# Kernel tuning notes

Hardware: AMD Instinct MI355X
Metric: run time of the kernel (lower is better)

The kernel has to match this reference:

```python
import jax, jax.numpy as jnp
import numpy as np

D = 1024       # d_model
H = 16         # num_heads
DK = D // H    # head dim (64)
DFF = 4096     # SwiGLU hidden dim
THETA = 10000.0
EPS = 1e-5
B, S = 2, 2048


def setup_inputs() -> dict:
    key = jax.random.key(0)
    ks = jax.random.split(key, 9)
    p = lambda k, shape: jax.random.normal(k, shape, dtype=jnp.float32) * 0.02
    return {
        "x": jax.random.normal(ks[0], (B, S, D), dtype=jnp.float32),
        "w_q": p(ks[1], (D, D)),   # Linear stores [out, in]
        "w_k": p(ks[2], (D, D)),
        "w_v": p(ks[3], (D, D)),
        "w_o": p(ks[4], (D, D)),
        "ln1_w": jnp.ones((D,), dtype=jnp.float32),
        "ln2_w": jnp.ones((D,), dtype=jnp.float32),
        "w1": p(ks[5], (DFF, D)),  # gate-in proj: d_model -> dff
        "w2": p(ks[6], (D, DFF)),  # down proj:    dff -> d_model
        "w3": p(ks[7], (DFF, D)),  # up proj:      d_model -> dff
    }


def _rmsnorm(x, w):
    xf = x.astype(jnp.float32)
    inv = jax.lax.rsqrt(jnp.mean(xf * xf, axis=-1, keepdims=True) + EPS)
    return (inv * xf * w).astype(x.dtype)


def _rope(x, pos):
    # x: [..., seq, DK]; pos: [seq]
    inv_freq = THETA ** (-(jnp.arange(0, DK, 2, dtype=jnp.float32) / DK))  # [DK/2]
    ang = pos.astype(jnp.float32)[:, None] * inv_freq                      # [seq, DK/2]
    cos, sin = jnp.cos(ang), jnp.sin(ang)
    xe, xo = x[..., ::2], x[..., 1::2]
    re = cos * xe - sin * xo
    ro = sin * xe + cos * xo
    return jnp.stack((re, ro), axis=-1).reshape(x.shape)  # interleave even/odd


def reference(x, w_q, w_k, w_v, w_o, ln1_w, ln2_w, w1, w2, w3):
    b, s, d = x.shape
    pos = jnp.arange(s)

    # --- attention sublayer ---
    h = _rmsnorm(x, ln1_w)
    def proj(w):  # [b,s,d] x [d,d] -> [b,H,s,DK]
        return jnp.einsum('bsd,ed->bse', h, w).reshape(b, s, H, DK).transpose(0, 2, 1, 3)
    q = _rope(proj(w_q), pos)
    k = _rope(proj(w_k), pos)
    v = proj(w_v)

    scores = jnp.einsum('bhqd,bhkd->bhqk', q, k) / (DK ** 0.5)
    causal = jnp.tril(jnp.ones((s, s), dtype=bool))
    scores = jnp.where(causal, scores, -jnp.inf)
    attn = jax.nn.softmax(scores, axis=-1)
    o = jnp.einsum('bhqk,bhkd->bhqd', attn, v).transpose(0, 2, 1, 3).reshape(b, s, d)
    x = x + jnp.einsum('bsd,ed->bse', o, w_o)

    # --- SwiGLU FFN sublayer ---
    h2 = _rmsnorm(x, ln2_w)
    u = jnp.einsum('bsd,fd->bsf', h2, w1)
    g = jnp.einsum('bsd,fd->bsf', h2, w3)
    ffn = jnp.einsum('bsf,df->bsd', u * jax.nn.sigmoid(u) * g, w2)
    return x + ffn
```

## Files before the change

### kernel.cpp

```cpp
#include <hip/hip_runtime.h>

typedef _Float16 half_t;
typedef _Float16 f16x8 __attribute__((ext_vector_type(8)));
typedef _Float16 f16x4 __attribute__((ext_vector_type(4)));
typedef _Float16 f16x2 __attribute__((ext_vector_type(2)));
typedef float fx4 __attribute__((ext_vector_type(4)));

typedef __attribute__((address_space(1))) const unsigned int as1_cuint;
typedef __attribute__((address_space(3))) unsigned int as3_uint;

__device__ __forceinline__ void gld16(const void* g, void* l) {
    __builtin_amdgcn_global_load_lds((as1_cuint*)g, (as3_uint*)l, 16, 0, 0);
}

template<int MODE>
__global__ __launch_bounds__(256, 2)
void gemm_bt(const half_t* __restrict__ A,
             const half_t* __restrict__ B0, const half_t* __restrict__ B1,
             const half_t* __restrict__ B2,
             half_t* o0, half_t* o1, half_t* o2, half_t* o3,
             int M, int N, int K)
{
    __shared__ half_t sA[128 * 32];
    __shared__ half_t sB[128 * 32];
    const int tid = threadIdx.x;
    const int wid = tid >> 6, lane = tid & 63;
    const int lm = lane & 15, lg = lane >> 4;
    const int wr = wid >> 1, wc = wid & 1;
    const int m0 = blockIdx.x * 128, n0 = blockIdx.y * 128;

    const half_t* Bp = B0;
    half_t* outb = o0;
    if (MODE == 1) {
        if (blockIdx.z == 1) { Bp = B1; outb = o1; }
        else if (blockIdx.z == 2) { Bp = B2; outb = o2; }
    }
    if (MODE == 4) {
        if (blockIdx.z == 1) outb = o1;
        else if (blockIdx.z == 2) outb = o2;
        else if (blockIdx.z == 3) outb = o3;
    }

    int Keff = K, koff = 0;
    if (MODE == 4) { Keff = K / gridDim.z; koff = blockIdx.z * Keff; }

    const int srow = tid >> 2;
    const int scolb = ((tid & 3) ^ ((srow >> 1) & 3)) << 4;
    const char* gA = (const char*)(A + (size_t)(m0 + srow) * K + koff) + scolb;
    const char* gB = (const char*)(Bp + (size_t)(n0 + srow) * K + koff) + scolb;
    const size_t rstep = (size_t)64 * K * sizeof(half_t);
    char* lA = (char*)sA + tid * 16;
    char* lB = (char*)sB + tid * 16;

    const int ksw = (lm >> 1) & 3;

    fx4 acc[4][4] = {};

    for (int kt = 0; kt < Keff; kt += 32) {
        gld16(gA, lA);
        gld16(gA + rstep, lA + 4096);
        gld16(gB, lB);
        gld16(gB + rstep, lB + 4096);
        gA += 64; gB += 64;
        __syncthreads();
        f16x8 aF[4], bF[4];
#pragma unroll
        for (int mi = 0; mi < 4; mi++)
            aF[mi] = *(const f16x8*)(sA + (wr * 64 + mi * 16 + lm) * 32 + (lg ^ ksw) * 8);
#pragma unroll
        for (int ni = 0; ni < 4; ni++)
            bF[ni] = *(const f16x8*)(sB + (wc * 64 + ni * 16 + lm) * 32 + (lg ^ ksw) * 8);
#pragma unroll
        for (int mi = 0; mi < 4; mi++)
#pragma unroll
            for (int ni = 0; ni < 4; ni++)
                acc[mi][ni] = __builtin_amdgcn_mfma_f32_16x16x32_f16(aF[mi], bF[ni], acc[mi][ni], 0, 0, 0);
        __syncthreads();
    }

#pragma unroll
    for (int mi = 0; mi < 4; mi++) {
#pragma unroll
        for (int ni = 0; ni < 4; ni++) {
#pragma unroll
            for (int r = 0; r < 4; r++) {
                int m = m0 + wr * 64 + mi * 16 + lg * 4 + r;
                int n = n0 + wc * 64 + ni * 16 + lm;
                float v = acc[mi][ni][r];
                size_t idx = (size_t)m * N + n;
                if (MODE == 1) {
                    int b = m >> 11, s = m & 2047, hh = n >> 6, dk = n & 63;
                    if (blockIdx.z == 2) {
                        outb[((size_t)(b * 16 + hh) * 64 + dk) * 2048 + s] = (half_t)v;
                    } else {
                        float pv = __shfl_xor(v, 1);
                        float f = __expf((float)(dk >> 1) * -0.28782313662f);
                        float c, sn;
                        __sincosf((float)s * f, &sn, &c);
                        float xe = (lm & 1) ? pv : v;
                        float xo = (lm & 1) ? v : pv;
                        float rv = (lm & 1) ? (sn * xe + c * xo) : (c * xe - sn * xo);
                        if (blockIdx.z == 0) rv *= 0.125f;
                        outb[((size_t)(b * 16 + hh) * 2048 + s) * 64 + dk] = (half_t)rv;
                    }
                } else {
                    outb[idx] = (half_t)v;
                }
            }
        }
    }
}

#define L256(buf, half, sec) (lbase + (buf) * 65536 + (half) * 16384 + (sec) * 8192)

#define KT256(CUR)                                                            \
  {                                                                           \
    const int BO = (CUR) * 65536;                                             \
    const int st1 = (t < nt - 1), st2 = (t < nt - 2);                         \
    const int s1 = (t + 1) * 128, s2 = (t + 2) * 128;                         \
    f16x8 aLo[4][2], aHi[4][2], bA[2][2], bB[2][2];                           \
                                         \
    _Pragma("unroll") for (int mi = 0; mi < 4; mi++) {                        \
        aLo[mi][0] = *(const f16x8*)(aBase + BO + mi * 2048 + swz0);          \
        aLo[mi][1] = *(const f16x8*)(aBase + BO + mi * 2048 + swz1);          \
    }                                                                         \
    _Pragma("unroll") for (int ni = 0; ni < 2; ni++) {                        \
        bA[ni][0] = *(const f16x8*)(bBase + BO + ni * 2048 + swz0);           \
        bA[ni][1] = *(const f16x8*)(bBase + BO + ni * 2048 + swz1);           \
    }                                                                         \
    if (st1) { gld16(pB10 + s1, L256(1 - (CUR), 3, 0));                       \
               gld16(pB1h + s1, L256(1 - (CUR), 3, 1)); }                     \
    asm volatile("s_waitcnt lgkmcnt(8)" ::: "memory");                        \
    __builtin_amdgcn_s_barrier();                                             \
    asm volatile("s_waitcnt lgkmcnt(0)" ::: "memory");                        \
    __builtin_amdgcn_sched_barrier(0);                                        \
    __builtin_amdgcn_s_setprio(1);                                            \
    _Pragma("unroll") for (int kk = 0; kk < 2; kk++)                          \
      _Pragma("unroll") for (int mi = 0; mi < 4; mi++)                        \
        _Pragma("unroll") for (int ni = 0; ni < 2; ni++)                      \
          acc[mi][ni] = __builtin_amdgcn_mfma_f32_16x16x32_f16(aLo[mi][kk], bA[ni][kk], acc[mi][ni], 0, 0, 0); \
    __builtin_amdgcn_s_setprio(0);                                            \
    __builtin_amdgcn_s_barrier();                                             \
                                         \
    _Pragma("unroll") for (int ni = 0; ni < 2; ni++) {                        \
        bB[ni][0] = *(const f16x8*)(bBase + BO + (2 + ni) * 2048 + swz0);     \
        bB[ni][1] = *(const f16x8*)(bBase + BO + (2 + ni) * 2048 + swz1);     \
    }                                                                         \
    if (st2) { gld16(pA00 + s2, L256(CUR, 0, 0)); }                           \
    __builtin_amdgcn_s_barrier();                                             \
    asm volatile("s_waitcnt lgkmcnt(0)" ::: "memory");                        \
    __builtin_amdgcn_sched_barrier(0);                                        \
    __builtin_amdgcn_s_setprio(1);                                            \
    _Pragma("unroll") for (int kk = 0; kk < 2; kk++)                          \
      _Pragma("unroll") for (int mi = 0; mi < 4; mi++)                        \
        _Pragma("unroll") for (int ni = 0; ni < 2; ni++)                      \
          acc[mi][2 + ni] = __builtin_amdgcn_mfma_f32_16x16x32_f16(aLo[mi][kk], bB[ni][kk], acc[mi][2 + ni], 0, 0, 0); \
    __builtin_amdgcn_s_setprio(0);                                            \
    __builtin_amdgcn_s_barrier();                                             \
                                         \
    _Pragma("unroll") for (int mi = 0; mi < 4; mi++) {                        \
        aHi[mi][0] = *(const f16x8*)(aBase + BO + (4 + mi) * 2048 + swz0);    \
        aHi[mi][1] = *(const f16x8*)(aBase + BO + (4 + mi) * 2048 + swz1);    \
    }                                                                         \
    if (st2) { gld16(pB00 + s2, L256(CUR, 2, 0));                             \
               gld16(pB0h + s2, L256(CUR, 2, 1)); }                           \
    __builtin_amdgcn_s_barrier();                                             \
    asm volatile("s_waitcnt lgkmcnt(0)" ::: "memory");                        \
    __builtin_amdgcn_sched_barrier(0);                                        \
    __builtin_amdgcn_s_setprio(1);                                            \
    _Pragma("unroll") for (int kk = 0; kk < 2; kk++)                          \
      _Pragma("unroll") for (int mi = 0; mi < 4; mi++)                        \
        _Pragma("unroll") for (int ni = 0; ni < 2; ni++)                      \
          acc[4 + mi][2 + ni] = __builtin_amdgcn_mfma_f32_16x16x32_f16(aHi[mi][kk], bB[ni][kk], acc[4 + mi][2 + ni], 0, 0, 0); \
    __builtin_amdgcn_s_setprio(0);                                            \
    __builtin_amdgcn_s_barrier();                                             \
                                         \
    if (st2) { gld16(pA0h + s2, L256(CUR, 0, 1));                             \
               gld16(pA10 + s2, L256(CUR, 1, 0));                             \
               gld16(pA1h + s2, L256(CUR, 1, 1)); }                           \
    __builtin_amdgcn_s_barrier();                                             \
    __builtin_amdgcn_sched_barrier(0);                                        \
    __builtin_amdgcn_s_setprio(1);                                            \
    _Pragma("unroll") for (int kk = 0; kk < 2; kk++)                          \
      _Pragma("unroll") for (int mi = 0; mi < 4; mi++)                        \
        _Pragma("unroll") for (int ni = 0; ni < 2; ni++)                      \
          acc[4 + mi][ni] = __builtin_amdgcn_mfma_f32_16x16x32_f16(aHi[mi][kk], bA[ni][kk], acc[4 + mi][ni], 0, 0, 0); \
    __builtin_amdgcn_s_setprio(0);                                            \
    if (t < nt - 2)       { asm volatile("s_waitcnt vmcnt(6)" ::: "memory"); }\
    else if (t == nt - 2) { asm volatile("s_waitcnt vmcnt(0)" ::: "memory"); }\
    __builtin_amdgcn_s_barrier();                                             \
  }

#define PRO256()                                                              \
    gld16(pA00, L256(0, 0, 0));                                               \
    gld16(pB00, L256(0, 2, 0)); gld16(pB0h, L256(0, 2, 1));                   \
    gld16(pA0h, L256(0, 0, 1)); gld16(pA10, L256(0, 1, 0)); gld16(pA1h, L256(0, 1, 1)); \
    gld16(pB10, L256(0, 3, 0)); gld16(pB1h, L256(0, 3, 1));                   \
    gld16(pA00 + 128, L256(1, 0, 0));                                         \
    gld16(pB00 + 128, L256(1, 2, 0)); gld16(pB0h + 128, L256(1, 2, 1));       \
    gld16(pA0h + 128, L256(1, 0, 1)); gld16(pA10 + 128, L256(1, 1, 0)); gld16(pA1h + 128, L256(1, 1, 1)); \
    asm volatile("s_waitcnt vmcnt(6)" ::: "memory");                          \
    __builtin_amdgcn_s_barrier();

__global__ __launch_bounds__(512, 2)
void gemm_dual9(const half_t* __restrict__ A,
                const half_t* __restrict__ B1, const half_t* __restrict__ B2,
                half_t* __restrict__ out, int M, int N, int K)
{
    __shared__ half_t smem[65536];
    const int tid = threadIdx.x;
    const int wid = tid >> 6, lane = tid & 63;
    const int lm = lane & 15, lg = lane >> 4;
    const int wr = wid >> 2, wc = wid & 3;
    const int flat = blockIdx.x + (blockIdx.y << 4);
    const int wg = (flat & 7) * 64 + (flat >> 3);
    const int m0 = (wg & 15) * 256, n0 = (wg >> 4) * 128;

    const size_t KB = (size_t)K * 2;
    const int srow = tid >> 3;
    const int schunk = (tid & 7) ^ (srow & 7);
    const char* pA  = (const char*)A  + (size_t)(m0 + srow) * KB + schunk * 16;
    const char* pB0 = (const char*)B1 + (size_t)(n0 + srow) * KB + schunk * 16;
    const char* pB1 = (const char*)B2 + (size_t)(n0 + srow) * KB + schunk * 16;
    const char* pA00 = pA;
    const char* pA0h = pA + 64 * KB;
    const char* pA10 = pA + 128 * KB;
    const char* pA1h = pA + 192 * KB;
    const char* pB00 = pB0;
    const char* pB0h = pB0 + 64 * KB;
    const char* pB10 = pB1;
    const char* pB1h = pB1 + 64 * KB;
    const int nt = 16;

    char* const lbase = (char*)smem + tid * 16;

    const int swz0 = ((lg ^ (lm & 7)) << 4);
    const int swz1 = (((4 + lg) ^ (lm & 7)) << 4);
    const char* aBase = (const char*)smem + wr * 16384 + lm * 128;
    const char* bBase = (const char*)smem + (2 + (wc >> 1)) * 16384 + (wc & 1) * 8192 + lm * 128;

    PRO256()

    fx4 acc[8][4] = {};

#pragma unroll 1
    for (int tt = 0; tt < 16; tt += 2) {
        { const int t = tt;     KT256(0) }
        { const int t = tt + 1; KT256(1) }
    }

    float* gb = (float*)smem;
    if (wc >= 2) {
        const int gw = wr * 2 + (wc - 2);
#pragma unroll
        for (int mi = 0; mi < 8; mi++)
#pragma unroll
            for (int ni = 0; ni < 4; ni++)
                *(fx4*)((char*)gb + ((((gw * 8 + mi) * 4 + ni) * 64 + lane) << 4)) = acc[mi][ni];
    }
    __syncthreads();
    if (wc < 2) {
        const int gw = wr * 2 + wc;
#pragma unroll
        for (int mi = 0; mi < 8; mi++)
#pragma unroll
            for (int ni = 0; ni < 4; ni++) {
                fx4 gv = *(const fx4*)((const char*)gb + ((((gw * 8 + mi) * 4 + ni) * 64 + lane) << 4));
#pragma unroll
                for (int r = 0; r < 4; r++) {
                    int m = m0 + wr * 128 + mi * 16 + lg * 4 + r;
                    int n = n0 + wc * 64 + ni * 16 + lm;
                    float u = acc[mi][ni][r], g = gv[r];
                    out[(size_t)m * N + n] = (half_t)(u / (1.f + __expf(-u)) * g);
                }
            }
    }
}

__global__ __launch_bounds__(256, 4)
void addnorm_k(const float* __restrict__ x,
               const half_t* __restrict__ p0, const half_t* __restrict__ p1,
               const float* __restrict__ w,
               float* __restrict__ outF, half_t* __restrict__ outH)
{
    int row = blockIdx.x * 4 + (threadIdx.x >> 6);
    int lane = threadIdx.x & 63;
    const float4* xr = (const float4*)(x + (size_t)row * 1024);
    const f16x4* p0r = (const f16x4*)(p0 + (size_t)row * 1024);
    const f16x4* p1r = (const f16x4*)(p1 + (size_t)row * 1024);
    float4 v[4];
    float s = 0.f;
#pragma unroll
    for (int i = 0; i < 4; i++) {
        float4 xv = xr[lane + 64 * i];
        f16x4 a0 = p0r[lane + 64 * i];
        f16x4 a1 = p1r[lane + 64 * i];
        v[i].x = xv.x + (float)a0[0] + (float)a1[0];
        v[i].y = xv.y + (float)a0[1] + (float)a1[1];
        v[i].z = xv.z + (float)a0[2] + (float)a1[2];
        v[i].w = xv.w + (float)a0[3] + (float)a1[3];
        s += v[i].x * v[i].x + v[i].y * v[i].y + v[i].z * v[i].z + v[i].w * v[i].w;
    }
#pragma unroll
    for (int o = 32; o > 0; o >>= 1) s += __shfl_xor(s, o);
    float inv = rsqrtf(s * (1.f / 1024.f) + 1e-5f);
    const float4* w4 = (const float4*)w;
    float4* oF = (float4*)(outF + (size_t)row * 1024);
    f16x4* oH = (f16x4*)(outH + (size_t)row * 1024);
#pragma unroll
    for (int i = 0; i < 4; i++) {
        oF[lane + 64 * i] = v[i];
        float4 wv = w4[lane + 64 * i];
        f16x4 ov = { (half_t)(v[i].x * inv * wv.x), (half_t)(v[i].y * inv * wv.y),
                     (half_t)(v[i].z * inv * wv.z), (half_t)(v[i].w * inv * wv.w) };
        oH[lane + 64 * i] = ov;
    }
}

__global__ __launch_bounds__(256, 8)
void reduce4_k(const half_t* __restrict__ p0, const half_t* __restrict__ p1,
               const half_t* __restrict__ p2, const half_t* __restrict__ p3,
               float* __restrict__ out, int n4)
{
    int i = blockIdx.x * 256 + threadIdx.x;
    if (i >= n4) return;
    float4 b = ((const float4*)out)[i];
    f16x4 a0 = ((const f16x4*)p0)[i];
    f16x4 a1 = ((const f16x4*)p1)[i];
    f16x4 a2 = ((const f16x4*)p2)[i];
    f16x4 a3 = ((const f16x4*)p3)[i];
    float4 o = { b.x + (float)a0[0] + (float)a1[0] + (float)a2[0] + (float)a3[0],
                 b.y + (float)a0[1] + (float)a1[1] + (float)a2[1] + (float)a3[1],
                 b.z + (float)a0[2] + (float)a1[2] + (float)a2[2] + (float)a3[2],
                 b.w + (float)a0[3] + (float)a1[3] + (float)a2[3] + (float)a3[3] };
    ((float4*)out)[i] = o;
}

struct CastA { const float* s; half_t* d; int n4; };
struct CastArgs { CastA a[7]; };

__global__ __launch_bounds__(256)
void cast_rms_k(CastArgs ca, const float* __restrict__ x,
                const float* __restrict__ w, half_t* __restrict__ out)
{
    if (blockIdx.y < 7) {
        CastA a = ca.a[blockIdx.y];
        int i = blockIdx.x * 256 + threadIdx.x;
        if (i >= a.n4) return;
        float4 v = ((const float4*)a.s)[i];
        ((f16x4*)a.d)[i] = (f16x4){ (half_t)v.x, (half_t)v.y, (half_t)v.z, (half_t)v.w };
        return;
    }
    if (blockIdx.x >= 1024) return;
    int row = blockIdx.x * 4 + (threadIdx.x >> 6);
    int lane = threadIdx.x & 63;
    const float4* xr = (const float4*)(x + (size_t)row * 1024);
    float4 v[4];
    float s = 0.f;
#pragma unroll
    for (int i = 0; i < 4; i++) {
        v[i] = xr[lane + 64 * i];
        s += v[i].x * v[i].x + v[i].y * v[i].y + v[i].z * v[i].z + v[i].w * v[i].w;
    }
#pragma unroll
    for (int o = 32; o > 0; o >>= 1) s += __shfl_xor(s, o);
    float inv = rsqrtf(s * (1.f / 1024.f) + 1e-5f);
    const float4* w4 = (const float4*)w;
    f16x4* o4 = (f16x4*)(out + (size_t)row * 1024);
#pragma unroll
    for (int i = 0; i < 4; i++) {
        float4 wv = w4[lane + 64 * i];
        f16x4 ov = { (half_t)(v[i].x * inv * wv.x), (half_t)(v[i].y * inv * wv.y),
                     (half_t)(v[i].z * inv * wv.z), (half_t)(v[i].w * inv * wv.w) };
        o4[lane + 64 * i] = ov;
    }
}

__global__ __launch_bounds__(256, 2)
void attn_k(const half_t* __restrict__ Q, const half_t* __restrict__ K,
            const half_t* __restrict__ VT, half_t* __restrict__ O)
{
    __shared__ half_t sK[2][128 * 64];
    __shared__ half_t sVT[2][64 * 128];
    __shared__ half_t sP[4][16 * 128];
    const int tid = threadIdx.x, wid = tid >> 6, lane = tid & 63;
    const int lm = lane & 15, lg = lane >> 4;
    const int flat = blockIdx.x + (blockIdx.y << 4);
    const int wg = (flat & 7) * 64 + (flat >> 3);
    const int p = wg & 15, bh = wg >> 4;
    const int b = bh >> 4, hh = bh & 15;
    const size_t base = (size_t)bh * (2048 * 64);

    const int krow = tid >> 3;
    const int kcsw = ((tid & 7) ^ (krow & 7)) << 4;
    const int vrow = tid >> 4;
    const int vcsw = ((tid & 15) ^ (vrow & 15)) << 4;
    const char* gK = (const char*)(K + base);
    const char* gV = (const char*)(VT + base);
    half_t* sPw = sP[wid];

    f16x8 vone;
#pragma unroll
    for (int j = 0; j < 8; j++) vone[j] = (half_t)1.f;

    for (int ph = 0; ph < 2; ph++) {
        const int qt = ph ? (31 - p) : p;
        const int q0 = qt * 64 + wid * 16;
        const int nT = (qt + 2) >> 1;

        f16x8 bQ[2];
#pragma unroll
        for (int ki = 0; ki < 2; ki++)
            bQ[ki] = *(const f16x8*)(Q + base + (size_t)(q0 + lm) * 64 + ki * 32 + lg * 8);

        fx4 oacc[4] = {};
        fx4 lacc = {};

        {
            char* lK = (char*)sK[0] + tid * 16;
            char* lV = (char*)sVT[0] + tid * 16;
#pragma unroll
            for (int i = 0; i < 4; i++)
                gld16(gK + (size_t)(i * 32 + krow) * 128 + kcsw, lK + i * 4096);
#pragma unroll
            for (int i = 0; i < 4; i++)
                gld16(gV + (size_t)(i * 16 + vrow) * 4096 + vcsw, lV + i * 4096);
        }
        __syncthreads();

        for (int t = 0; t < nT; t++) {
            const int cur = t & 1;
            if (t + 1 < nT) {
                const int kv1 = (t + 1) * 128;
                char* lK = (char*)sK[cur ^ 1] + tid * 16;
                char* lV = (char*)sVT[cur ^ 1] + tid * 16;
#pragma unroll
                for (int i = 0; i < 4; i++)
                    gld16(gK + (size_t)(kv1 + i * 32 + krow) * 128 + kcsw, lK + i * 4096);
#pragma unroll
                for (int i = 0; i < 4; i++)
                    gld16(gV + (size_t)(i * 16 + vrow) * 4096 + (size_t)kv1 * 2 + vcsw, lV + i * 4096);
            }
            const half_t* cK = sK[cur];
            const half_t* cVT = sVT[cur];
            const int kv0 = t * 128;

            fx4 st[8] = {};
#pragma unroll
            for (int ki = 0; ki < 2; ki++) {
#pragma unroll
                for (int mi = 0; mi < 8; mi++) {
                    f16x8 aK = *(const f16x8*)(cK + ((mi * 16 + lm) << 6) +
                                               (((ki * 4 + lg) ^ (lm & 7)) << 3));
                    st[mi] = __builtin_amdgcn_mfma_f32_16x16x32_f16(aK, bQ[ki], st[mi], 0, 0, 0);
                }
            }

            const bool diag = (t == nT - 1);
            const int qg = q0 + lm;
#pragma unroll
            for (int mi = 0; mi < 8; mi++) {
                f16x4 ev;
#pragma unroll
                for (int r = 0; r < 4; r++) {
                    float e = __expf(st[mi][r]);
                    if (diag && (kv0 + mi * 16 + lg * 4 + r > qg)) e = 0.f;
                    ev[r] = (half_t)e;
                }
                *(f16x4*)(sPw + (lm << 7) +
                          ((((mi * 2 + (lg >> 1)) ^ lm) << 3) | ((lg & 1) << 2))) = ev;
            }

#pragma unroll
            for (int k2 = 0; k2 < 4; k2++) {
                f16x8 aP = *(const f16x8*)(sPw + (lm << 7) + (((k2 * 4 + lg) ^ lm) << 3));
#pragma unroll
                for (int ni = 0; ni < 4; ni++) {
                    f16x8 bV = *(const f16x8*)(cVT + ((ni * 16 + lm) << 7) +
                                               (((k2 * 4 + lg) ^ lm) << 3));
                    oacc[ni] = __builtin_amdgcn_mfma_f32_16x16x32_f16(aP, bV, oacc[ni], 0, 0, 0);
                }
                lacc = __builtin_amdgcn_mfma_f32_16x16x32_f16(aP, vone, lacc, 0, 0, 0);
            }
            __syncthreads();
        }

        float inv[4];
#pragma unroll
        for (int r = 0; r < 4; r++) inv[r] = 1.f / lacc[r];
#pragma unroll
        for (int ni = 0; ni < 4; ni++)
#pragma unroll
            for (int r = 0; r < 4; r++) {
                int s = q0 + lg * 4 + r;
                O[((size_t)b * 2048 + s) * 1024 + hh * 64 + ni * 16 + lm] =
                    (half_t)(oacc[ni][r] * inv[r]);
            }
    }
}

extern "C" void kernel_launch(void* const* d_in, const int* in_sizes, int n_in,
                              void* d_out, int out_size, void* d_ws, size_t ws_size,
                              hipStream_t stream)
{
    const float* x   = (const float*)d_in[0];
    const float* wq  = (const float*)d_in[1];
    const float* wk  = (const float*)d_in[2];
    const float* wv  = (const float*)d_in[3];
    const float* wo  = (const float*)d_in[4];
    const float* ln1 = (const float*)d_in[5];
    const float* ln2 = (const float*)d_in[6];
    const float* w1  = (const float*)d_in[7];
    const float* w2  = (const float*)d_in[8];
    const float* w3  = (const float*)d_in[9];

    half_t* W = (half_t*)d_ws;
    const size_t Mi = 1048576;
    half_t* wq16 = W;
    half_t* wk16 = W + Mi;
    half_t* wv16 = W + 2 * Mi;
    half_t* wo16 = W + 3 * Mi;
    half_t* w116 = W + 4 * Mi;
    half_t* w316 = W + 8 * Mi;
    half_t* w216 = W + 12 * Mi;
    half_t* h16  = W + 16 * Mi;
    half_t* q16  = W + 20 * Mi;
    half_t* k16  = W + 24 * Mi;
    half_t* vt16 = W + 28 * Mi;
    half_t* a16  = W + 16 * Mi;
    half_t* h216 = W + 32 * Mi;
    half_t* P0   = W + 20 * Mi;
    half_t* P1   = W + 24 * Mi;
    half_t* D0   = W;
    half_t* D1   = W + 4 * Mi;
    half_t* D2   = W + 8 * Mi;
    half_t* D3   = W + 36 * Mi;

    CastArgs ca;
    ca.a[0] = { wq, wq16, 262144 };
    ca.a[1] = { wk, wk16, 262144 };
    ca.a[2] = { wv, wv16, 262144 };
    ca.a[3] = { wo, wo16, 262144 };
    ca.a[4] = { w1, w116, 1048576 };
    ca.a[5] = { w2, w216, 1048576 };
    ca.a[6] = { w3, w316, 1048576 };

    cast_rms_k<<<dim3(4096, 8), 256, 0, stream>>>(ca, x, ln1, h16);
    gemm_bt<1><<<dim3(32, 8, 3), 256, 0, stream>>>(h16, wq16, wk16, wv16,
                                                   q16, k16, vt16, nullptr,
                                                   4096, 1024, 1024);
    attn_k<<<dim3(16, 32), 256, 0, stream>>>(q16, k16, vt16, h16);
    gemm_bt<4><<<dim3(32, 8, 2), 256, 0, stream>>>(h16, wo16, nullptr, nullptr,
                                                   P0, P1, nullptr, nullptr,
                                                   4096, 1024, 1024);
    addnorm_k<<<dim3(1024), 256, 0, stream>>>(x, P0, P1, ln2,
                                              (float*)d_out, h216);
    gemm_dual9<<<dim3(16, 32), 512, 0, stream>>>(h216, w116, w316, a16,
                                                 4096, 4096, 1024);
    gemm_bt<4><<<dim3(32, 8, 4), 256, 0, stream>>>(a16, w216, nullptr, nullptr,
                                                   D0, D1, D2, D3,
                                                   4096, 1024, 4096);
    reduce4_k<<<dim3(4096), 256, 0, stream>>>(D0, D1, D2, D3, (float*)d_out, 1048576);
    (void)in_sizes; (void)n_in; (void)out_size; (void)ws_size;
}
```

Measured before the change: 363.7 us.

## Run both causal query tiles concurrently in 512-thread attention blocks sharing K/V tiles

The attention kernel now runs eight waves per block. Waves 0-3 handle the short query tile p and waves 4-7 handle the paired long tile 31-p, all at once instead of in two sequential phases. K/V tiles loaded into shared memory are shared by both halves, so K/V global traffic per block roughly halves. V is now single-buffered and loaded after an extra barrier, and waves for the short tile sit idle once their tiles run out. The added syncs, idle waves and loss of V double-buffering may offset the saving.

Result: slower. 372.5 us (+2.4%).

```diff
diff --git a/kernel.cpp b/kernel.cpp
--- a/kernel.cpp
+++ b/kernel.cpp
@@ -376,13 +376,13 @@
     }
 }
 
-__global__ __launch_bounds__(256, 2)
+__global__ __launch_bounds__(512, 4)
 void attn_k(const half_t* __restrict__ Q, const half_t* __restrict__ K,
             const half_t* __restrict__ VT, half_t* __restrict__ O)
 {
     __shared__ half_t sK[2][128 * 64];
-    __shared__ half_t sVT[2][64 * 128];
-    __shared__ half_t sP[4][16 * 128];
+    __shared__ half_t sVT[64 * 128];
+    __shared__ half_t sP[8][16 * 128];
     const int tid = threadIdx.x, wid = tid >> 6, lane = tid & 63;
     const int lm = lane & 15, lg = lane >> 4;
     const int flat = blockIdx.x + (blockIdx.y << 4);
@@ -391,6 +391,11 @@
     const int b = bh >> 4, hh = bh & 15;
     const size_t base = (size_t)bh * (2048 * 64);
 
+    const int qt = (wid < 4) ? p : (31 - p);
+    const int q0 = qt * 64 + (wid & 3) * 16;
+    const int nTs = (qt + 2) >> 1;
+    const int nTL = (33 - p) >> 1;
+
     const int krow = tid >> 3;
     const int kcsw = ((tid & 7) ^ (krow & 7)) << 4;
     const int vrow = tid >> 4;
@@ -403,48 +408,40 @@
 #pragma unroll
     for (int j = 0; j < 8; j++) vone[j] = (half_t)1.f;
 
-    for (int ph = 0; ph < 2; ph++) {
-        const int qt = ph ? (31 - p) : p;
-        const int q0 = qt * 64 + wid * 16;
-        const int nT = (qt + 2) >> 1;
-
-        f16x8 bQ[2];
-#pragma unroll
-        for (int ki = 0; ki < 2; ki++)
-            bQ[ki] = *(const f16x8*)(Q + base + (size_t)(q0 + lm) * 64 + ki * 32 + lg * 8);
-
-        fx4 oacc[4] = {};
-        fx4 lacc = {};
-
-        {
-            char* lK = (char*)sK[0] + tid * 16;
-            char* lV = (char*)sVT[0] + tid * 16;
-#pragma unroll
-            for (int i = 0; i < 4; i++)
-                gld16(gK + (size_t)(i * 32 + krow) * 128 + kcsw, lK + i * 4096);
-#pragma unroll
-            for (int i = 0; i < 4; i++)
-                gld16(gV + (size_t)(i * 16 + vrow) * 4096 + vcsw, lV + i * 4096);
+    f16x8 bQ[2];
+#pragma unroll
+    for (int ki = 0; ki < 2; ki++)
+        bQ[ki] = *(const f16x8*)(Q + base + (size_t)(q0 + lm) * 64 + ki * 32 + lg * 8);
+
+    fx4 oacc[4] = {};
+    fx4 lacc = {};
+
+    {
+        char* lK = (char*)sK[0] + tid * 16;
+        char* lV = (char*)sVT + tid * 16;
+#pragma unroll
+        for (int i = 0; i < 2; i++)
+            gld16(gK + (size_t)(i * 64 + krow) * 128 + kcsw, lK + i * 8192);
+#pragma unroll
+        for (int i = 0; i < 2; i++)
+            gld16(gV + (size_t)(i * 32 + vrow) * 4096 + vcsw, lV + i * 8192);
+    }
+    __syncthreads();
+
+    for (int t = 0; t < nTL; t++) {
+        const int cur = t & 1;
+        if (t + 1 < nTL) {
+            const int kv1 = (t + 1) * 128;
+            char* lK = (char*)sK[cur ^ 1] + tid * 16;
+#pragma unroll
+            for (int i = 0; i < 2; i++)
+                gld16(gK + (size_t)(kv1 + i * 64 + krow) * 128 + kcsw, lK + i * 8192);
         }
-        __syncthreads();
-
-        for (int t = 0; t < nT; t++) {
-            const int cur = t & 1;
-            if (t + 1 < nT) {
-                const int kv1 = (t + 1) * 128;
-                char* lK = (char*)sK[cur ^ 1] + tid * 16;
-                char* lV = (char*)sVT[cur ^ 1] + tid * 16;
-#pragma unroll
-                for (int i = 0; i < 4; i++)
-                    gld16(gK + (size_t)(kv1 + i * 32 + krow) * 128 + kcsw, lK + i * 4096);
-#pragma unroll
-                for (int i = 0; i < 4; i++)
-                    gld16(gV + (size_t)(i * 16 + vrow) * 4096 + (size_t)kv1 * 2 + vcsw, lV + i * 4096);
-            }
+        const int kv0 = t * 128;
+        const bool act = (t < nTs);
+
+        if (act) {
             const half_t* cK = sK[cur];
-            const half_t* cVT = sVT[cur];
-            const int kv0 = t * 128;
-
             fx4 st[8] = {};
 #pragma unroll
             for (int ki = 0; ki < 2; ki++) {
@@ -455,8 +452,7 @@
                     st[mi] = __builtin_amdgcn_mfma_f32_16x16x32_f16(aK, bQ[ki], st[mi], 0, 0, 0);
                 }
             }
-
-            const bool diag = (t == nT - 1);
+            const bool diag = (t == nTs - 1);
             const int qg = q0 + lm;
 #pragma unroll
             for (int mi = 0; mi < 8; mi++) {
@@ -470,33 +466,42 @@
                 *(f16x4*)(sPw + (lm << 7) +
                           ((((mi * 2 + (lg >> 1)) ^ lm) << 3) | ((lg & 1) << 2))) = ev;
             }
-
+        }
+        __syncthreads();
+        if (act) {
 #pragma unroll
             for (int k2 = 0; k2 < 4; k2++) {
                 f16x8 aP = *(const f16x8*)(sPw + (lm << 7) + (((k2 * 4 + lg) ^ lm) << 3));
 #pragma unroll
                 for (int ni = 0; ni < 4; ni++) {
-                    f16x8 bV = *(const f16x8*)(cVT + ((ni * 16 + lm) << 7) +
+                    f16x8 bV = *(const f16x8*)(sVT + ((ni * 16 + lm) << 7) +
                                                (((k2 * 4 + lg) ^ lm) << 3));
                     oacc[ni] = __builtin_amdgcn_mfma_f32_16x16x32_f16(aP, bV, oacc[ni], 0, 0, 0);
                 }
                 lacc = __builtin_amdgcn_mfma_f32_16x16x32_f16(aP, vone, lacc, 0, 0, 0);
             }
-            __syncthreads();
         }
-
-        float inv[4];
-#pragma unroll
-        for (int r = 0; r < 4; r++) inv[r] = 1.f / lacc[r];
-#pragma unroll
-        for (int ni = 0; ni < 4; ni++)
-#pragma unroll
-            for (int r = 0; r < 4; r++) {
-                int s = q0 + lg * 4 + r;
-                O[((size_t)b * 2048 + s) * 1024 + hh * 64 + ni * 16 + lm] =
-                    (half_t)(oacc[ni][r] * inv[r]);
-            }
-    }
+        __syncthreads();
+        if (t + 1 < nTL) {
+            const int kv1 = (t + 1) * 128;
+            char* lV = (char*)sVT + tid * 16;
+#pragma unroll
+            for (int i = 0; i < 2; i++)
+                gld16(gV + (size_t)(i * 32 + vrow) * 4096 + (size_t)kv1 * 2 + vcsw, lV + i * 8192);
+        }
+    }
+
+    float inv[4];
+#pragma unroll
+    for (int r = 0; r < 4; r++) inv[r] = 1.f / lacc[r];
+#pragma unroll
+    for (int ni = 0; ni < 4; ni++)
+#pragma unroll
+        for (int r = 0; r < 4; r++) {
+            int s = q0 + lg * 4 + r;
+            O[((size_t)b * 2048 + s) * 1024 + hh * 64 + ni * 16 + lm] =
+                (half_t)(oacc[ni][r] * inv[r]);
+        }
 }
 
 extern "C" void kernel_launch(void* const* d_in, const int* in_sizes, int n_in,
@@ -549,7 +554,7 @@
     gemm_bt<1><<<dim3(32, 8, 3), 256, 0, stream>>>(h16, wq16, wk16, wv16,
                                                    q16, k16, vt16, nullptr,
                                                    4096, 1024, 1024);
-    attn_k<<<dim3(16, 32), 256, 0, stream>>>(q16, k16, vt16, h16);
+    attn_k<<<dim3(16, 32), 512, 0, stream>>>(q16, k16, vt16, h16);
     gemm_bt<4><<<dim3(32, 8, 2), 256, 0, stream>>>(h16, wo16, nullptr, nullptr,
                                                    P0, P1, nullptr, nullptr,
                                                    4096, 1024, 1024);
```
